# Performance work log

Measured on AMD Instinct MI355X. Metric: run time of the kernel, lower is better.

The kernel has to match this reference:

```python
import jax, jax.numpy as jnp
import numpy as np

N_NODES = 8192
N_EDGES = 49152
IN_F, HID, H1, H2, OUT_F = 128, 64, 64, 5, 32
N_BONDS = 64


def setup_inputs() -> dict:
    key = jax.random.key(0)
    ks = jax.random.split(key, 12)
    s = 0.05
    return {
        "x": jax.random.normal(ks[0], (N_NODES, IN_F), jnp.float32),
        "edge_index": jax.random.randint(ks[1], (2, N_EDGES), 0, N_NODES, jnp.int32),
        "lefts": jax.random.randint(ks[2], (N_BONDS,), 0, N_NODES, jnp.int32),
        "rights": jax.random.randint(ks[3], (N_BONDS,), 0, N_NODES, jnp.int32),
        "W1": jax.random.normal(ks[4], (H1 * HID, IN_F), jnp.float32) * s,
        "att_src1": jax.random.normal(ks[5], (H1, HID), jnp.float32) * s,
        "att_dst1": jax.random.normal(ks[6], (H1, HID), jnp.float32) * s,
        "b1": jnp.zeros((H1 * HID,), jnp.float32),
        "W2": jax.random.normal(ks[7], (H2 * OUT_F, H1 * HID), jnp.float32) * s,
        "att_src2": jax.random.normal(ks[8], (H2, OUT_F), jnp.float32) * s,
        "att_dst2": jax.random.normal(ks[9], (H2, OUT_F), jnp.float32) * s,
        "b2": jnp.zeros((OUT_F,), jnp.float32),
    }


def _gat_conv(x, src, dst, W, a_src, a_dst, b, concat):
    # x: [N, F_in]; W: [H*C, F_in]; a_src/a_dst: [H, C]
    N = x.shape[0]
    H, C = a_src.shape
    h = (x @ W.T).reshape(N, H, C)                    # [N, H, C]
    alpha_s = jnp.einsum("nhc,hc->nh", h, a_src)      # [N, H]
    alpha_d = jnp.einsum("nhc,hc->nh", h, a_dst)
    logits = jax.nn.leaky_relu(alpha_s[src] + alpha_d[dst], negative_slope=0.2)  # [E, H]
    # scatter-softmax over incoming edges of each destination node
    m = jax.ops.segment_max(logits, dst, num_segments=N)
    e = jnp.exp(logits - m[dst])
    denom = jax.ops.segment_sum(e, dst, num_segments=N)
    alpha = e / denom[dst]                            # [E, H]
    msg = h[src] * alpha[:, :, None]                  # [E, H, C]
    out = jax.ops.segment_sum(msg, dst, num_segments=N)  # [N, H, C]
    out = out.reshape(N, H * C) if concat else out.mean(axis=1)
    return out + b


def reference(x, edge_index, lefts, rights, W1, att_src1, att_dst1, b1,
              W2, att_src2, att_dst2, b2):
    N = x.shape[0]
    loops = jnp.arange(N, dtype=edge_index.dtype)
    src = jnp.concatenate([edge_index[0], loops])
    dst = jnp.concatenate([edge_index[1], loops])
    x1 = jax.nn.elu(_gat_conv(x, src, dst, W1, att_src1, att_dst1, b1, concat=True))
    x2 = _gat_conv(x1, src, dst, W2, att_src2, att_dst2, b2, concat=False)  # [N, OUT_F]
    score = (x2[lefts] + x2[rights]).sum(axis=-1)     # [N_BONDS]
    return jax.nn.softmax(score, axis=0)
```

## Files before the change

kernel.cpp:

```cpp
#include <hip/hip_runtime.h>
#include <hip/hip_bf16.h>
#include <math.h>

#define N_NODES  8192
#define N_EDGES  49152
#define E_TOT    57344
#define IN_F     128
#define HID      64
#define NH1      64
#define NH2      5
#define OUT_F    32
#define F1       4096
#define F2       160
#define N_BONDS  64
#define ET       16
#define NP       4
#define HG       16

typedef short bf16x8 __attribute__((ext_vector_type(8)));
typedef float f32x4  __attribute__((ext_vector_type(4)));

__device__ __forceinline__ float lrelu(float x){ return x > 0.f ? x : 0.2f*x; }

__device__ __forceinline__ unsigned short bf16_rne(float f){
    unsigned u = __float_as_uint(f);
    unsigned r = u + 0x7FFF + ((u >> 16) & 1);
    return (unsigned short)(r >> 16);
}
__device__ __forceinline__ float bf16f(unsigned short h){
    return __uint_as_float((unsigned)h << 16);
}

__device__ __forceinline__ void block_sync_lds(){
    asm volatile("s_waitcnt lgkmcnt(0)" ::: "memory");
    __builtin_amdgcn_s_barrier();
    asm volatile("" ::: "memory");
}

__device__ __forceinline__ void gload_lds16(const unsigned short* gp, unsigned short* lp_base){
    __builtin_amdgcn_global_load_lds(
        (const __attribute__((address_space(1))) unsigned int*)(const void*)gp,
        (__attribute__((address_space(3))) unsigned int*)(void*)lp_base,
        16, 0, 0);
}

__global__ void k_count(const int* __restrict__ ei, int* counts){
    int i = blockIdx.x*256 + threadIdx.x;
    if (i < N_EDGES) atomicAdd(&counts[ei[N_EDGES + i]], 1);
}
__global__ __launch_bounds__(1024) void k_scan(const int* __restrict__ counts,
                                               int* __restrict__ row_start,
                                               int* __restrict__ cursor){
    __shared__ int sd[1024];
    int t = threadIdx.x;
    int v[8]; int sum = 0;
    #pragma unroll
    for (int i=0;i<8;i++){ v[i] = counts[t*8+i] + 1; sum += v[i]; }
    sd[t] = sum; __syncthreads();
    for (int off=1; off<1024; off<<=1){
        int vv = (t >= off) ? sd[t-off] : 0;
        __syncthreads();
        sd[t] += vv;
        __syncthreads();
    }
    int run = sd[t] - sum;
    #pragma unroll
    for (int i=0;i<8;i++){ row_start[t*8+i] = run; cursor[t*8+i] = run; run += v[i]; }
    if (t == 1023) row_start[N_NODES] = run;
}
__global__ void k_fill(const int* __restrict__ ei, int* cursor, int* __restrict__ csr_src){
    int i = blockIdx.x*256 + threadIdx.x;
    if (i >= E_TOT) return;
    int s, d;
    if (i < N_EDGES){ s = ei[i]; d = ei[N_EDGES + i]; }
    else { s = i - N_EDGES; d = s; }
    int pos = atomicAdd(&cursor[d], 1);
    csr_src[pos] = s;
}

__global__ void k_packw1d(const float* __restrict__ W1,
                          unsigned short* __restrict__ fh, unsigned short* __restrict__ fl){
    int g = blockIdx.x*256 + threadIdx.x;
    int lane = g & 63, ct = (g >> 6) & 3, ks = (g >> 8) & 3, hg = g >> 10;
    int col = hg*64 + ct*16 + (lane & 15);
    int k = ks*32 + (lane >> 4)*8;
    const float* src = W1 + (size_t)col*IN_F + k;
    bf16x8 hv, lv;
    #pragma unroll
    for (int j=0;j<8;j++){
        float f = src[j];
        unsigned short hb = bf16_rne(f);
        hv[j] = (short)hb;
        lv[j] = (short)bf16_rne(f - bf16f(hb));
    }
    *(bf16x8*)(fh + (size_t)g*8) = hv;
    *(bf16x8*)(fl + (size_t)g*8) = lv;
}

__global__ void k_packw2d(const float* __restrict__ W2,
                          unsigned short* __restrict__ fh, unsigned short* __restrict__ fl){
    int g = blockIdx.x*256 + threadIdx.x;
    int lane = g & 63, ni = (g >> 6) % 10, kc = g / 640;
    int n = ni*16 + (lane & 15);
    int k = kc*32 + (lane >> 4)*8;
    const float* src = W2 + (size_t)n*F1 + k;
    bf16x8 hv, lv;
    #pragma unroll
    for (int j=0;j<8;j++){
        float f = src[j];
        unsigned short hb = bf16_rne(f);
        hv[j] = (short)hb;
        lv[j] = (short)bf16_rne(f - bf16f(hb));
    }
    *(bf16x8*)(fh + (size_t)g*8) = hv;
    *(bf16x8*)(fl + (size_t)g*8) = lv;
}

__global__ __launch_bounds__(128) void k_attvec(const float* __restrict__ W1,
        const float* __restrict__ a_s, const float* __restrict__ a_d,
        float* __restrict__ vsT, float* __restrict__ vdT){
    int h = blockIdx.x, k = threadIdx.x;
    float s = 0.f, d = 0.f;
    for (int c = 0; c < HID; c++){
        float w = W1[(size_t)(h*HID + c)*IN_F + k];
        s += a_s[h*HID + c] * w;
        d += a_d[h*HID + c] * w;
    }
    vsT[k*NH1 + h] = s;
    vdT[k*NH1 + h] = d;
}

__global__ __launch_bounds__(128) void k_alpha1x(const float* __restrict__ x,
        const float* __restrict__ vsT, const float* __restrict__ vdT,
        float* __restrict__ as1, float* __restrict__ ad1){
    int n = blockIdx.x, t = threadIdx.x;
    __shared__ float xs[IN_F];
    xs[t] = x[(size_t)n*IN_F + t];
    __syncthreads();
    if (t < NH1){
        float s = 0.f, d = 0.f;
        for (int k = 0; k < IN_F; k++){
            float xv = xs[k];
            s += xv * vsT[k*NH1 + t];
            d += xv * vdT[k*NH1 + t];
        }
        as1[n*NH1 + t] = s;
        ad1[n*NH1 + t] = d;
    }
}

__global__ __launch_bounds__(256) void k_aggx64(const float* __restrict__ x,
        const float* __restrict__ as1, const float* __restrict__ ad1,
        const int* __restrict__ row_start, const int* __restrict__ csr_src,
        unsigned short* __restrict__ txhi){
    int n = blockIdx.x, t = threadIdx.x;
    __shared__ float ad_s[NH1];
    __shared__ float wt[ET][NH1];
    __shared__ int   st[ET];
    __shared__ float xs[ET][IN_F];
    int e0 = row_start[n], e1 = row_start[n+1];
    if (t < NH1) ad_s[t] = ad1[n*NH1 + t];
    int hq = t >> 4, f0 = (t & 15)*8;
    float acc[4][8] = {};
    float D[4] = {0.f, 0.f, 0.f, 0.f};
    for (int eb = e0; eb < e1; eb += ET){
        int ne = min(ET, e1 - eb);
        if (t < ne) st[t] = csr_src[eb + t];
        __syncthreads();
        for (int idx = t; idx < ne*32; idx += 256){
            int e = idx >> 5, f4 = idx & 31;
            *(float4*)&xs[e][f4*4] = *(const float4*)(x + (size_t)st[e]*IN_F + f4*4);
        }
        for (int idx = t; idx < ne*NH1; idx += 256){
            int e = idx >> 6, hh = idx & 63;
            wt[e][hh] = __expf(lrelu(as1[st[e]*NH1 + hh] + ad_s[hh]));
        }
        __syncthreads();
        for (int e = 0; e < ne; e++){
            float4 v0 = *(const float4*)&xs[e][f0];
            float4 v1 = *(const float4*)&xs[e][f0+4];
            float xv[8] = {v0.x,v0.y,v0.z,v0.w,v1.x,v1.y,v1.z,v1.w};
            #pragma unroll
            for (int c=0;c<4;c++){
                float w = wt[e][hq*4 + c];
                D[c] += w;
                #pragma unroll
                for (int j=0;j<8;j++) acc[c][j] += w*xv[j];
            }
        }
        __syncthreads();
    }
    #pragma unroll
    for (int c=0;c<4;c++){
        float dinv = 1.f / D[c];
        bf16x8 hv;
        #pragma unroll
        for (int j=0;j<8;j++) hv[j] = (short)bf16_rne(acc[c][j] * dinv);
        size_t o = ((size_t)(hq*4 + c)*N_NODES + n)*IN_F + f0;
        *(bf16x8*)(txhi + o) = hv;
    }
}

__global__ __launch_bounds__(512, 4) void k_gemm12(
        const unsigned short* __restrict__ txhi,
        const unsigned short* __restrict__ w1fh, const unsigned short* __restrict__ w1fl,
        const unsigned short* __restrict__ w2fh, const unsigned short* __restrict__ w2fl,
        const float* __restrict__ b1,
        float* __restrict__ P){
    __shared__ __attribute__((aligned(16))) unsigned short Als[8192];
    __shared__ __attribute__((aligned(16))) unsigned short W1sh[8192];
    __shared__ __attribute__((aligned(16))) unsigned short W2s[20480];
    __shared__ __attribute__((aligned(16))) unsigned short X1s[4096];

    const int tid  = threadIdx.x;
    const int wave = tid >> 6, lane = tid & 63;
    const int wr = wave & 1, wc = wave >> 1;
    const int q = lane >> 4, l16 = lane & 15;
    const int row0 = blockIdx.x * 64;
    const int g = blockIdx.y;
    const int h0 = g * HG;
    const int nbase = (wc < 2) ? wc*3 : 6 + (wc-2)*2;

    {
        const unsigned short* Ab = txhi + ((size_t)h0*N_NODES + row0)*IN_F;
        const unsigned short* W1b = w1fh + (size_t)h0*8192;
        #pragma unroll
        for (int j=0;j<2;j++){
            int idx = j*8 + wave;
            int eo = idx*512 + lane*8;
            int row = eo >> 7;
            int se = (eo & ~127) | ((eo & 127) ^ ((row & 7) << 3));
            gload_lds16(Ab + se, &Als[idx*512]);
        }
        #pragma unroll
        for (int j=0;j<2;j++){
            int idx = j*8 + wave;
            gload_lds16(W1b + idx*512 + lane*8, &W1sh[idx*512]);
        }
    }

    f32x4 acc2[2][3] = {};
    bf16x8 wlo[4];

    #pragma unroll 1
    for (int hh = 0; hh < HG; hh++){
        const int h = h0 + hh;
        block_sync_lds();
        {
            const unsigned short* W1lb = w1fl + (size_t)h*8192;
            #pragma unroll
            for (int ks=0;ks<4;ks++)
                wlo[ks] = *(const bf16x8*)(W1lb + (size_t)(ks*4 + wc)*512 + lane*8);
        }
        asm volatile("" ::: "memory");
        {
            const unsigned short* W2bh = w2fh + (size_t)h*10240;
            const unsigned short* W2bl = w2fl + (size_t)h*10240;
            #pragma unroll
            for (int j=0;j<5;j++){
                int idx = j*8 + wave;
                const unsigned short* src = (idx < 20) ? (W2bh + idx*512 + lane*8)
                                                       : (W2bl + (idx-20)*512 + lane*8);
                gload_lds16(src, &W2s[idx*512]);
            }
        }
        asm volatile("s_waitcnt vmcnt(9)" ::: "memory");
        __builtin_amdgcn_s_barrier();
        f32x4 c1[2] = {};
        __builtin_amdgcn_s_setprio(1);
        #pragma unroll
        for (int ks=0;ks<4;ks++){
            bf16x8 bh = *(const bf16x8*)&W1sh[(ks*4 + wc)*512 + lane*8];
            #pragma unroll
            for (int mi=0;mi<2;mi++){
                int arow = wr*32 + mi*16 + l16;
                int sidx = (arow*128 + ks*32 + q*8) ^ ((arow & 7) << 3);
                bf16x8 af = *(const bf16x8*)&Als[sidx];
                c1[mi] = __builtin_amdgcn_mfma_f32_16x16x32_bf16(af, bh, c1[mi], 0,0,0);
                c1[mi] = __builtin_amdgcn_mfma_f32_16x16x32_bf16(af, wlo[ks], c1[mi], 0,0,0);
            }
        }
        __builtin_amdgcn_s_setprio(0);
        {
            int col = wc*16 + l16;
            float b = b1[h*64 + col];
            #pragma unroll
            for (int mi=0;mi<2;mi++){
                #pragma unroll
                for (int i=0;i<4;i++){
                    float v = c1[mi][i] + b;
                    float o = v > 0.f ? v : (__expf(v) - 1.f);
                    int row = wr*32 + mi*16 + q*4 + i;
                    int sidx = (row*64 + col) ^ ((row & 7) << 3);
                    X1s[sidx] = bf16_rne(o);
                }
            }
        }
        asm volatile("s_waitcnt vmcnt(0) lgkmcnt(0)" ::: "memory");
        __builtin_amdgcn_s_barrier();
        if (hh + 1 < HG){
            const unsigned short* Ab = txhi + ((size_t)(h+1)*N_NODES + row0)*IN_F;
            const unsigned short* W1b = w1fh + (size_t)(h+1)*8192;
            #pragma unroll
            for (int j=0;j<2;j++){
                int idx = j*8 + wave;
                int eo = idx*512 + lane*8;
                int row = eo >> 7;
                int se = (eo & ~127) | ((eo & 127) ^ ((row & 7) << 3));
                gload_lds16(Ab + se, &Als[idx*512]);
            }
            #pragma unroll
            for (int j=0;j<2;j++){
                int idx = j*8 + wave;
                gload_lds16(W1b + idx*512 + lane*8, &W1sh[idx*512]);
            }
        }
        __builtin_amdgcn_s_setprio(1);
        #pragma unroll
        for (int ks=0;ks<2;ks++){
            bf16x8 a2[2];
            #pragma unroll
            for (int mi=0;mi<2;mi++){
                int row = wr*32 + mi*16 + l16;
                int sidx = (row*64 + ks*32 + q*8) ^ ((row & 7) << 3);
                a2[mi] = *(const bf16x8*)&X1s[sidx];
            }
            if (wc < 2){
                #pragma unroll
                for (int ni=0;ni<3;ni++){
                    int f = (ks*10 + nbase + ni)*512 + lane*8;
                    bf16x8 bh = *(const bf16x8*)&W2s[f];
                    bf16x8 bl = *(const bf16x8*)&W2s[10240 + f];
                    #pragma unroll
                    for (int mi=0;mi<2;mi++){
                        acc2[mi][ni] = __builtin_amdgcn_mfma_f32_16x16x32_bf16(a2[mi], bh, acc2[mi][ni], 0,0,0);
                        acc2[mi][ni] = __builtin_amdgcn_mfma_f32_16x16x32_bf16(a2[mi], bl, acc2[mi][ni], 0,0,0);
                    }
                }
            } else {
                #pragma unroll
                for (int ni=0;ni<2;ni++){
                    int f = (ks*10 + nbase + ni)*512 + lane*8;
                    bf16x8 bh = *(const bf16x8*)&W2s[f];
                    bf16x8 bl = *(const bf16x8*)&W2s[10240 + f];
                    #pragma unroll
                    for (int mi=0;mi<2;mi++){
                        acc2[mi][ni] = __builtin_amdgcn_mfma_f32_16x16x32_bf16(a2[mi], bh, acc2[mi][ni], 0,0,0);
                        acc2[mi][ni] = __builtin_amdgcn_mfma_f32_16x16x32_bf16(a2[mi], bl, acc2[mi][ni], 0,0,0);
                    }
                }
            }
        }
        __builtin_amdgcn_s_setprio(0);
    }

    float* outp = P + ((size_t)g*N_NODES + row0)*F2;
    #pragma unroll
    for (int mi=0;mi<2;mi++)
        #pragma unroll
        for (int ni=0;ni<3;ni++){
            if (wc >= 2 && ni >= 2) continue;
            #pragma unroll
            for (int i=0;i<4;i++){
                int rr = wr*32 + mi*16 + q*4 + i;
                int cc = (nbase + ni)*16 + l16;
                outp[(size_t)rr*F2 + cc] = acc2[mi][ni][i];
            }
        }
}

__global__ __launch_bounds__(256) void k_redalpha(const float* __restrict__ P,
        const float* __restrict__ att_s, const float* __restrict__ att_d,
        float* __restrict__ h2, float* __restrict__ as2, float* __restrict__ ad2){
    __shared__ float hs[64][164];
    __shared__ float avs[160], avd[160];
    int b = blockIdx.x, t = threadIdx.x;
    int n0 = b*64;
    if (t < 160){ avs[t] = att_s[t]; avd[t] = att_d[t]; }
    const int NV = N_NODES*F2/4;
    int base = b * (64*F2/4);
    #pragma unroll
    for (int v=0; v<10; v++){
        int i = base + v*256 + t;
        float4 a = ((const float4*)P)[i];
        #pragma unroll
        for (int kb=1; kb<NP; kb++){
            float4 bb = ((const float4*)P)[(size_t)kb*NV + i];
            a.x+=bb.x; a.y+=bb.y; a.z+=bb.z; a.w+=bb.w;
        }
        ((float4*)h2)[i] = a;
        int flat = (v*256 + t)*4;
        int n = flat / F2, c = flat % F2;
        *(float4*)&hs[n][c] = a;
    }
    __syncthreads();
    for (int idx = t; idx < 320; idx += 256){
        int n = idx/5, hh = idx%5;
        const float* hp = &hs[n][hh*32];
        const float* ap = &avs[hh*32];
        const float* dp = &avd[hh*32];
        float s=0.f, d=0.f;
        #pragma unroll
        for (int c=0;c<32;c++){ float hv=hp[c]; s += hv*ap[c]; d += hv*dp[c]; }
        as2[(n0+n)*NH2 + hh] = s;
        ad2[(n0+n)*NH2 + hh] = d;
    }
}

__global__ __launch_bounds__(256) void k_agg2(const float* __restrict__ h2,
        const float* __restrict__ as2, const float* __restrict__ ad2,
        const int* __restrict__ row_start, const int* __restrict__ csr_src,
        const float* __restrict__ b2, float* __restrict__ x2){
    int n = blockIdx.x, t = threadIdx.x;
    __shared__ float ad_s[NH2], den_s[NH2], sacc[F2];
    int e0 = row_start[n], e1 = row_start[n+1];
    if (t < NH2) ad_s[t] = ad2[n*NH2 + t];
    __syncthreads();
    if (t < NH2){
        float d = 0.f;
        for (int e=e0;e<e1;e++){
            int s = csr_src[e];
            d += __expf(lrelu(as2[s*NH2 + t] + ad_s[t]));
        }
        den_s[t] = d;
    }
    __syncthreads();
    if (t < F2){
        int h = t >> 5;
        float adh  = ad_s[h];
        float dinv = 1.f/den_s[h];
        float acc = 0.f;
        for (int e=e0;e<e1;e++){
            int s = csr_src[e];
            float w = __expf(lrelu(as2[s*NH2 + h] + adh)) * dinv;
            acc += w * h2[(size_t)s*F2 + t];
        }
        sacc[t] = acc;
    }
    __syncthreads();
    if (t < OUT_F){
        float v = (sacc[t] + sacc[t+32] + sacc[t+64] + sacc[t+96] + sacc[t+128]) * 0.2f + b2[t];
        x2[n*OUT_F + t] = v;
    }
}

__global__ __launch_bounds__(64) void k_bond(const float* __restrict__ x2,
        const int* __restrict__ lefts, const int* __restrict__ rights,
        float* __restrict__ out){
    int b = threadIdx.x;
    int L = lefts[b], R = rights[b];
    float s = 0.f;
    #pragma unroll
    for (int c=0;c<OUT_F;c+=4){
        float4 l4 = *(const float4*)(x2 + (size_t)L*OUT_F + c);
        float4 r4 = *(const float4*)(x2 + (size_t)R*OUT_F + c);
        s += l4.x+l4.y+l4.z+l4.w + r4.x+r4.y+r4.z+r4.w;
    }
    float m = s;
    #pragma unroll
    for (int off=1; off<64; off<<=1) m = fmaxf(m, __shfl_xor(m, off));
    float e = expf(s - m);
    float sum = e;
    #pragma unroll
    for (int off=1; off<64; off<<=1) sum += __shfl_xor(sum, off);
    out[b] = e / sum;
}

extern "C" void kernel_launch(void* const* d_in, const int* in_sizes, int n_in,
                              void* d_out, int out_size, void* d_ws, size_t ws_size,
                              hipStream_t stream){
    const float* x      = (const float*)d_in[0];
    const int*   ei     = (const int*)  d_in[1];
    const int*   lefts  = (const int*)  d_in[2];
    const int*   rights = (const int*)  d_in[3];
    const float* W1     = (const float*)d_in[4];
    const float* att_s1 = (const float*)d_in[5];
    const float* att_d1 = (const float*)d_in[6];
    const float* b1     = (const float*)d_in[7];
    const float* W2     = (const float*)d_in[8];
    const float* att_s2 = (const float*)d_in[9];
    const float* att_d2 = (const float*)d_in[10];
    const float* b2     = (const float*)d_in[11];
    float* out = (float*)d_out;

    char* ws = (char*)d_ws;
    size_t off = 0;
    auto alloc = [&](size_t bytes) -> void* {
        void* p = ws + off;
        off += (bytes + 255) & ~(size_t)255;
        return p;
    };
    unsigned short* txhi = (unsigned short*)alloc((size_t)NH1*N_NODES*IN_F*2);
    float* part   = (float*)alloc((size_t)NP*N_NODES*F2*4);
    float* h2     = (float*)alloc((size_t)N_NODES*F2*4);
    float* as1    = (float*)alloc((size_t)N_NODES*NH1*4);
    float* ad1    = (float*)alloc((size_t)N_NODES*NH1*4);
    float* as2    = (float*)alloc((size_t)N_NODES*NH2*4);
    float* ad2    = (float*)alloc((size_t)N_NODES*NH2*4);
    float* x2     = (float*)alloc((size_t)N_NODES*OUT_F*4);
    float* vsT    = (float*)alloc((size_t)IN_F*NH1*4);
    float* vdT    = (float*)alloc((size_t)IN_F*NH1*4);
    unsigned short* w1fh = (unsigned short*)alloc((size_t)F1*IN_F*2);
    unsigned short* w1fl = (unsigned short*)alloc((size_t)F1*IN_F*2);
    unsigned short* w2fh = (unsigned short*)alloc((size_t)128*10*512*2);
    unsigned short* w2fl = (unsigned short*)alloc((size_t)128*10*512*2);
    int* counts    = (int*)alloc((size_t)N_NODES*4);
    int* row_start = (int*)alloc((size_t)(N_NODES+1)*4);
    int* cursor    = (int*)alloc((size_t)N_NODES*4);
    int* csr_src   = (int*)alloc((size_t)E_TOT*4);

    hipMemsetAsync(counts, 0, (size_t)N_NODES*4, stream);
    k_count<<<192, 256, 0, stream>>>(ei, counts);
    k_scan<<<1, 1024, 0, stream>>>(counts, row_start, cursor);
    k_fill<<<224, 256, 0, stream>>>(ei, cursor, csr_src);

    k_packw1d<<<65536/256, 256, 0, stream>>>(W1, w1fh, w1fl);
    k_packw2d<<<81920/256, 256, 0, stream>>>(W2, w2fh, w2fl);

    k_attvec<<<NH1, 128, 0, stream>>>(W1, att_s1, att_d1, vsT, vdT);
    k_alpha1x<<<N_NODES, 128, 0, stream>>>(x, vsT, vdT, as1, ad1);

    k_aggx64<<<N_NODES, 256, 0, stream>>>(x, as1, ad1, row_start, csr_src, txhi);

    k_gemm12<<<dim3(128, NP), 512, 0, stream>>>(txhi, w1fh, w1fl, w2fh, w2fl, b1, part);
    k_redalpha<<<128, 256, 0, stream>>>(part, att_s2, att_d2, h2, as2, ad2);

    k_agg2<<<N_NODES, 256, 0, stream>>>(h2, as2, ad2, row_start, csr_src, b2, x2);

    k_bond<<<1, 64, 0, stream>>>(x2, lefts, rights, out);
}
```

Baseline: 241.8 us.

## Fuse weight-prep kernels, vectorize alpha1 projection, single-pass agg2 softmax

Merges the W1/W2 bf16 split-packing kernels and the attention-vector kernel into one launch, and transposes vsT/vdT so k_alpha1x can use all 128 threads with float4 loads. k_redalpha now uses 256 smaller blocks for more parallelism, and k_agg2 computes the softmax denominator in the same edge loop as the weighted sum, dropping a separate pass and a barrier. The goal is fewer launches and less redundant edge traversal, though each agg2 thread now recomputes exp for its own head.

After: 261.8 us. +8.3%, slower.

```diff
diff --git a/kernel.cpp b/kernel.cpp
--- a/kernel.cpp
+++ b/kernel.cpp
@@ -78,56 +78,57 @@
     csr_src[pos] = s;
 }
 
-__global__ void k_packw1d(const float* __restrict__ W1,
-                          unsigned short* __restrict__ fh, unsigned short* __restrict__ fl){
-    int g = blockIdx.x*256 + threadIdx.x;
-    int lane = g & 63, ct = (g >> 6) & 3, ks = (g >> 8) & 3, hg = g >> 10;
-    int col = hg*64 + ct*16 + (lane & 15);
-    int k = ks*32 + (lane >> 4)*8;
-    const float* src = W1 + (size_t)col*IN_F + k;
-    bf16x8 hv, lv;
-    #pragma unroll
-    for (int j=0;j<8;j++){
-        float f = src[j];
-        unsigned short hb = bf16_rne(f);
-        hv[j] = (short)hb;
-        lv[j] = (short)bf16_rne(f - bf16f(hb));
-    }
-    *(bf16x8*)(fh + (size_t)g*8) = hv;
-    *(bf16x8*)(fl + (size_t)g*8) = lv;
-}
-
-__global__ void k_packw2d(const float* __restrict__ W2,
-                          unsigned short* __restrict__ fh, unsigned short* __restrict__ fl){
-    int g = blockIdx.x*256 + threadIdx.x;
-    int lane = g & 63, ni = (g >> 6) % 10, kc = g / 640;
-    int n = ni*16 + (lane & 15);
-    int k = kc*32 + (lane >> 4)*8;
-    const float* src = W2 + (size_t)n*F1 + k;
-    bf16x8 hv, lv;
-    #pragma unroll
-    for (int j=0;j<8;j++){
-        float f = src[j];
-        unsigned short hb = bf16_rne(f);
-        hv[j] = (short)hb;
-        lv[j] = (short)bf16_rne(f - bf16f(hb));
-    }
-    *(bf16x8*)(fh + (size_t)g*8) = hv;
-    *(bf16x8*)(fl + (size_t)g*8) = lv;
-}
-
-__global__ __launch_bounds__(128) void k_attvec(const float* __restrict__ W1,
+__global__ __launch_bounds__(256) void k_prep(const float* __restrict__ W1,
+        const float* __restrict__ W2,
         const float* __restrict__ a_s, const float* __restrict__ a_d,
+        unsigned short* __restrict__ w1fh, unsigned short* __restrict__ w1fl,
+        unsigned short* __restrict__ w2fh, unsigned short* __restrict__ w2fl,
         float* __restrict__ vsT, float* __restrict__ vdT){
-    int h = blockIdx.x, k = threadIdx.x;
-    float s = 0.f, d = 0.f;
-    for (int c = 0; c < HID; c++){
-        float w = W1[(size_t)(h*HID + c)*IN_F + k];
-        s += a_s[h*HID + c] * w;
-        d += a_d[h*HID + c] * w;
-    }
-    vsT[k*NH1 + h] = s;
-    vdT[k*NH1 + h] = d;
+    int b = blockIdx.x, t = threadIdx.x;
+    if (b < 256){
+        int g = b*256 + t;
+        int lane = g & 63, ct = (g >> 6) & 3, ks = (g >> 8) & 3, hg = g >> 10;
+        int col = hg*64 + ct*16 + (lane & 15);
+        int k = ks*32 + (lane >> 4)*8;
+        const float* src = W1 + (size_t)col*IN_F + k;
+        bf16x8 hv, lv;
+        #pragma unroll
+        for (int j=0;j<8;j++){
+            float f = src[j];
+            unsigned short hb = bf16_rne(f);
+            hv[j] = (short)hb;
+            lv[j] = (short)bf16_rne(f - bf16f(hb));
+        }
+        *(bf16x8*)(w1fh + (size_t)g*8) = hv;
+        *(bf16x8*)(w1fl + (size_t)g*8) = lv;
+    } else if (b < 576){
+        int g = (b-256)*256 + t;
+        int lane = g & 63, ni = (g >> 6) % 10, kc = g / 640;
+        int n = ni*16 + (lane & 15);
+        int k = kc*32 + (lane >> 4)*8;
+        const float* src = W2 + (size_t)n*F1 + k;
+        bf16x8 hv, lv;
+        #pragma unroll
+        for (int j=0;j<8;j++){
+            float f = src[j];
+            unsigned short hb = bf16_rne(f);
+            hv[j] = (short)hb;
+            lv[j] = (short)bf16_rne(f - bf16f(hb));
+        }
+        *(bf16x8*)(w2fh + (size_t)g*8) = hv;
+        *(bf16x8*)(w2fl + (size_t)g*8) = lv;
+    } else {
+        int h = (b-576)*2 + (t >> 7);
+        int k = t & 127;
+        float s = 0.f, d = 0.f;
+        for (int c = 0; c < HID; c++){
+            float w = W1[(size_t)(h*HID + c)*IN_F + k];
+            s += a_s[h*HID + c] * w;
+            d += a_d[h*HID + c] * w;
+        }
+        vsT[h*IN_F + k] = s;
+        vdT[h*IN_F + k] = d;
+    }
 }
 
 __global__ __launch_bounds__(128) void k_alpha1x(const float* __restrict__ x,
@@ -137,16 +138,16 @@
     __shared__ float xs[IN_F];
     xs[t] = x[(size_t)n*IN_F + t];
     __syncthreads();
-    if (t < NH1){
-        float s = 0.f, d = 0.f;
-        for (int k = 0; k < IN_F; k++){
-            float xv = xs[k];
-            s += xv * vsT[k*NH1 + t];
-            d += xv * vdT[k*NH1 + t];
-        }
-        as1[n*NH1 + t] = s;
-        ad1[n*NH1 + t] = d;
-    }
+    int hd = t & 63;
+    const float* vp = ((t < 64) ? vsT : vdT) + (size_t)hd*IN_F;
+    float s = 0.f;
+    #pragma unroll
+    for (int k = 0; k < IN_F; k += 4){
+        float4 v = *(const float4*)(vp + k);
+        s += xs[k]*v.x + xs[k+1]*v.y + xs[k+2]*v.z + xs[k+3]*v.w;
+    }
+    if (t < 64) as1[n*NH1 + hd] = s;
+    else        ad1[n*NH1 + hd] = s;
 }
 
 __global__ __launch_bounds__(256) void k_aggx64(const float* __restrict__ x,
@@ -372,15 +373,15 @@
 __global__ __launch_bounds__(256) void k_redalpha(const float* __restrict__ P,
         const float* __restrict__ att_s, const float* __restrict__ att_d,
         float* __restrict__ h2, float* __restrict__ as2, float* __restrict__ ad2){
-    __shared__ float hs[64][164];
+    __shared__ float hs[32][164];
     __shared__ float avs[160], avd[160];
     int b = blockIdx.x, t = threadIdx.x;
-    int n0 = b*64;
+    int n0 = b*32;
     if (t < 160){ avs[t] = att_s[t]; avd[t] = att_d[t]; }
     const int NV = N_NODES*F2/4;
-    int base = b * (64*F2/4);
-    #pragma unroll
-    for (int v=0; v<10; v++){
+    int base = b * (32*F2/4);
+    #pragma unroll
+    for (int v=0; v<5; v++){
         int i = base + v*256 + t;
         float4 a = ((const float4*)P)[i];
         #pragma unroll
@@ -394,8 +395,8 @@
         *(float4*)&hs[n][c] = a;
     }
     __syncthreads();
-    for (int idx = t; idx < 320; idx += 256){
-        int n = idx/5, hh = idx%5;
+    if (t < 160){
+        int n = t/5, hh = t%5;
         const float* hp = &hs[n][hh*32];
         const float* ap = &avs[hh*32];
         const float* dp = &avd[hh*32];
@@ -407,35 +408,26 @@
     }
 }
 
-__global__ __launch_bounds__(256) void k_agg2(const float* __restrict__ h2,
+__global__ __launch_bounds__(192) void k_agg2(const float* __restrict__ h2,
         const float* __restrict__ as2, const float* __restrict__ ad2,
         const int* __restrict__ row_start, const int* __restrict__ csr_src,
         const float* __restrict__ b2, float* __restrict__ x2){
     int n = blockIdx.x, t = threadIdx.x;
-    __shared__ float ad_s[NH2], den_s[NH2], sacc[F2];
+    __shared__ float ad_s[NH2], sacc[F2];
     int e0 = row_start[n], e1 = row_start[n+1];
     if (t < NH2) ad_s[t] = ad2[n*NH2 + t];
     __syncthreads();
-    if (t < NH2){
-        float d = 0.f;
+    if (t < F2){
+        int h = t >> 5;
+        float adh = ad_s[h];
+        float acc = 0.f, D = 0.f;
         for (int e=e0;e<e1;e++){
             int s = csr_src[e];
-            d += __expf(lrelu(as2[s*NH2 + t] + ad_s[t]));
-        }
-        den_s[t] = d;
-    }
-    __syncthreads();
-    if (t < F2){
-        int h = t >> 5;
-        float adh  = ad_s[h];
-        float dinv = 1.f/den_s[h];
-        float acc = 0.f;
-        for (int e=e0;e<e1;e++){
-            int s = csr_src[e];
-            float w = __expf(lrelu(as2[s*NH2 + h] + adh)) * dinv;
+            float w = __expf(lrelu(as2[s*NH2 + h] + adh));
             acc += w * h2[(size_t)s*F2 + t];
-        }
-        sacc[t] = acc;
+            D += w;
+        }
+        sacc[t] = acc / D;
     }
     __syncthreads();
     if (t < OUT_F){
@@ -498,8 +490,8 @@
     float* as2    = (float*)alloc((size_t)N_NODES*NH2*4);
     float* ad2    = (float*)alloc((size_t)N_NODES*NH2*4);
     float* x2     = (float*)alloc((size_t)N_NODES*OUT_F*4);
-    float* vsT    = (float*)alloc((size_t)IN_F*NH1*4);
-    float* vdT    = (float*)alloc((size_t)IN_F*NH1*4);
+    float* vsT    = (float*)alloc((size_t)NH1*IN_F*4);
+    float* vdT    = (float*)alloc((size_t)NH1*IN_F*4);
     unsigned short* w1fh = (unsigned short*)alloc((size_t)F1*IN_F*2);
     unsigned short* w1fl = (unsigned short*)alloc((size_t)F1*IN_F*2);
     unsigned short* w2fh = (unsigned short*)alloc((size_t)128*10*512*2);
@@ -514,18 +506,17 @@
     k_scan<<<1, 1024, 0, stream>>>(counts, row_start, cursor);
     k_fill<<<224, 256, 0, stream>>>(ei, cursor, csr_src);
 
-    k_packw1d<<<65536/256, 256, 0, stream>>>(W1, w1fh, w1fl);
-    k_packw2d<<<81920/256, 256, 0, stream>>>(W2, w2fh, w2fl);
-
-    k_attvec<<<NH1, 128, 0, stream>>>(W1, att_s1, att_d1, vsT, vdT);
+    k_prep<<<608, 256, 0, stream>>>(W1, W2, att_s1, att_d1,
+                                    w1fh, w1fl, w2fh, w2fl, vsT, vdT);
+
     k_alpha1x<<<N_NODES, 128, 0, stream>>>(x, vsT, vdT, as1, ad1);
 
     k_aggx64<<<N_NODES, 256, 0, stream>>>(x, as1, ad1, row_start, csr_src, txhi);
 
     k_gemm12<<<dim3(128, NP), 512, 0, stream>>>(txhi, w1fh, w1fl, w2fh, w2fl, b1, part);
-    k_redalpha<<<128, 256, 0, stream>>>(part, att_s2, att_d2, h2, as2, ad2);
-
-    k_agg2<<<N_NODES, 256, 0, stream>>>(h2, as2, ad2, row_start, csr_src, b2, x2);
+    k_redalpha<<<256, 256, 0, stream>>>(part, att_s2, att_d2, h2, as2, ad2);
+
+    k_agg2<<<N_NODES, 192, 0, stream>>>(h2, as2, ad2, row_start, csr_src, b2, x2);
 
     k_bond<<<1, 64, 0, stream>>>(x2, lefts, rights, out);
 }
```
